# Kernel tuning notes

Hardware: AMD Instinct MI355X
Metric: run time of the kernel (lower is better)

## Reference

```python
import jax, jax.numpy as jnp
import numpy as np

HEADS = 16
DIM_HEAD = 64
LN_EPS = 1e-5
COS_EPS = 1e-8


def setup_inputs() -> dict:
    key = jax.random.key(0)
    ks = jax.random.split(key, 5)
    dim = 1024
    inner = HEADS * DIM_HEAD
    q = jax.random.normal(ks[0], (4, 1024, dim), dtype=jnp.float32)
    k = jax.random.normal(ks[1], (4, 2048, dim), dtype=jnp.float32)
    v = jax.random.normal(ks[2], (4, 2048, dim), dtype=jnp.float32)
    W_in = jax.random.normal(ks[3], (dim, inner), dtype=jnp.float32) * (1.0 / np.sqrt(dim))
    W_out = jax.random.normal(ks[4], (inner, dim), dtype=jnp.float32) * (1.0 / np.sqrt(inner))
    ln_gamma = jnp.ones((dim,), dtype=jnp.float32)
    ln_beta = jnp.zeros((dim,), dtype=jnp.float32)
    b_out = jnp.zeros((dim,), dtype=jnp.float32)
    return {"q": q, "k": k, "v": v, "ln_gamma": ln_gamma, "ln_beta": ln_beta,
            "W_in": W_in, "W_out": W_out, "b_out": b_out}


def _layernorm(x, gamma, beta):
    mu = jnp.mean(x, axis=-1, keepdims=True)
    var = jnp.mean(jnp.square(x - mu), axis=-1, keepdims=True)  # biased, as torch
    return (x - mu) * jax.lax.rsqrt(var + LN_EPS) * gamma + beta


def _project(t, gamma, beta, W_in):
    # LayerNorm -> Linear(no bias) -> split heads: b n (h d) -> b h n d
    x = _layernorm(t, gamma, beta) @ W_in
    b, n, _ = x.shape
    return x.reshape(b, n, HEADS, DIM_HEAD).transpose(0, 2, 1, 3)


def reference(q, k, v, ln_gamma, ln_beta, W_in, W_out, b_out):
    f_q = _project(q, ln_gamma, ln_beta, W_in)  # [b,h,n,d]
    f_k = _project(k, ln_gamma, ln_beta, W_in)  # [b,h,m,d]
    f_v = _project(v, ln_gamma, ln_beta, W_in)  # [b,h,m,d]
    dots = jnp.einsum('bhnd,bhmd->bhnm', f_q, f_k)
    qn = jnp.linalg.norm(f_q, axis=-1, keepdims=True)          # [b,h,n,1]
    kn = jnp.linalg.norm(f_k, axis=-1, keepdims=True)          # [b,h,m,1]
    attn = dots / (qn * kn.transpose(0, 1, 3, 2) + COS_EPS)    # [b,h,n,m]
    out = jnp.einsum('bhnm,bhmd->bhnd', attn, f_v)             # [b,h,n,d]
    b, h, n, d = out.shape
    out = out.transpose(0, 2, 1, 3).reshape(b, n, h * d)       # b n (h d)
    return out @ W_out + b_out
```

## Files before the change

### kernel.cpp

```cpp
#include <hip/hip_runtime.h>

constexpr int BATCH = 4;
constexpr int SEQQ  = 1024;
constexpr int SEQK  = 2048;
constexpr int DIM   = 1024;
constexpr int NH    = 16;
constexpr int DH    = 64;
constexpr int RQ    = BATCH * SEQQ;
constexpr int RK    = BATCH * SEQK;
constexpr int RTOT  = RQ + 2 * RK;
constexpr int BH    = BATCH * NH;
constexpr int NSLC  = 8;
constexpr float LN_EPS = 1e-5f;

typedef _Float16 f16;
typedef __attribute__((ext_vector_type(8))) _Float16 f16x8;
typedef __attribute__((ext_vector_type(4))) float f32x4;

__device__ __forceinline__ void async16(const void* g, void* l) {
  __builtin_amdgcn_global_load_lds(
      (const __attribute__((address_space(1))) void*)g,
      (__attribute__((address_space(3))) void*)l, 16, 0, 0);
}

__global__ void __launch_bounds__(256) ln_to_f16(
    const float* __restrict__ q, const float* __restrict__ k,
    const float* __restrict__ v, const float* __restrict__ gamma,
    const float* __restrict__ beta, f16* __restrict__ a_h) {
  const int row = blockIdx.x * 4 + (threadIdx.x >> 6);
  const int lane = threadIdx.x & 63;
  const float* src;
  if (row < RQ)            src = q + (size_t)row * DIM;
  else if (row < RQ + RK)  src = k + (size_t)(row - RQ) * DIM;
  else                     src = v + (size_t)(row - RQ - RK) * DIM;
  float4 x[4];
  float s = 0.f, s2 = 0.f;
#pragma unroll
  for (int c = 0; c < 4; c++) {
    x[c] = ((const float4*)src)[c * 64 + lane];
    s  += x[c].x + x[c].y + x[c].z + x[c].w;
    s2 += x[c].x * x[c].x + x[c].y * x[c].y + x[c].z * x[c].z + x[c].w * x[c].w;
  }
#pragma unroll
  for (int off = 1; off < 64; off <<= 1) {
    s  += __shfl_xor(s, off);
    s2 += __shfl_xor(s2, off);
  }
  const float mu = s / DIM;
  const float rs = rsqrtf(s2 / DIM - mu * mu + LN_EPS);
#pragma unroll
  for (int c = 0; c < 4; c++) {
    float4 g = ((const float4*)gamma)[c * 64 + lane];
    float4 b = ((const float4*)beta)[c * 64 + lane];
    union { f16 h[4]; uint2 u; } o;
    o.h[0] = (f16)((x[c].x - mu) * rs * g.x + b.x);
    o.h[1] = (f16)((x[c].y - mu) * rs * g.y + b.y);
    o.h[2] = (f16)((x[c].z - mu) * rs * g.z + b.z);
    o.h[3] = (f16)((x[c].w - mu) * rs * g.w + b.w);
    ((uint2*)(a_h + (size_t)row * DIM))[c * 64 + lane] = o.u;
  }
}

__global__ void __launch_bounds__(256) transpose_f16(
    const float* __restrict__ W0, const float* __restrict__ W1,
    f16* __restrict__ T0, f16* __restrict__ T1) {
  const float* W = blockIdx.z ? W1 : W0;
  f16* T = blockIdx.z ? T1 : T0;
  __shared__ float tile[32][33];
  int tx = threadIdx.x & 31, ty = threadIdx.x >> 5;
  int k0 = blockIdx.x * 32, n0 = blockIdx.y * 32;
#pragma unroll
  for (int i = 0; i < 4; i++)
    tile[ty + 8 * i][tx] = W[(size_t)(k0 + ty + 8 * i) * DIM + n0 + tx];
  __syncthreads();
#pragma unroll
  for (int i = 0; i < 4; i++)
    T[(size_t)(n0 + ty + 8 * i) * DIM + k0 + tx] = (f16)tile[tx][ty + 8 * i];
}

constexpr int PT_A = 320 * 64;
constexpr int PT_B = 256 * 64;

#define STAGE_A(buf, kt) do {                                        \
    const f16* s_ = gA + (size_t)(kt) * 64;                          \
    f16* d_ = AsW + (buf) * PT_A;                                    \
    async16(s_,          d_);                                        \
    async16(s_ +  65536, d_ + 4096);                                 \
    async16(s_ + 131072, d_ + 8192);                                 \
    async16(s_ + 196608, d_ + 12288);                                \
    async16(s_ + 262144, d_ + 16384);                                \
  } while (0)

#define STAGE_B(buf, kt) do {                                        \
    const f16* s_ = gB + (size_t)(kt) * 64;                          \
    f16* d_ = BsW + (buf) * PT_B;                                    \
    async16(s_,          d_);                                        \
    async16(s_ +  65536, d_ + 4096);                                 \
    async16(s_ + 131072, d_ + 8192);                                 \
    async16(s_ + 196608, d_ + 12288);                                \
  } while (0)

#define STAGE_AB(buf, kt) do { STAGE_A(buf, kt); STAGE_B(buf, kt); } while (0)

#define WT9 asm volatile("s_waitcnt vmcnt(9)" ::: "memory")
#define WT0 asm volatile("s_waitcnt vmcnt(0)" ::: "memory")
#define STN ((void)0)

#define HALF(BUF, H)                                                 \
    _Pragma("unroll") for (int j_ = 0; j_ < 4; ++j_)                 \
      bf[j_] = *(const f16x8*)(bB##H + (BUF) * PT_B + j_ * 1024);    \
    _Pragma("unroll") for (int f_ = 0; f_ < 5; ++f_)                 \
      af0[f_] = *(const f16x8*)(aB##H + (BUF) * PT_A + f_ * 1024);   \
    _Pragma("unroll") for (int f_ = 0; f_ < 5; ++f_)                 \
      af1[f_] = *(const f16x8*)(aB##H + (BUF) * PT_A + 5120 +        \
                                f_ * 1024);                          \
    __builtin_amdgcn_s_setprio(1);                                   \
    _Pragma("unroll") for (int f_ = 0; f_ < 5; ++f_)                 \
      _Pragma("unroll") for (int j_ = 0; j_ < 4; ++j_)               \
        acc[f_][j_] = __builtin_amdgcn_mfma_f32_16x16x32_f16(        \
            af0[f_], bf[j_], acc[f_][j_], 0, 0, 0);                  \
    _Pragma("unroll") for (int f_ = 0; f_ < 5; ++f_)                 \
      _Pragma("unroll") for (int j_ = 0; j_ < 4; ++j_)               \
        acc[5 + f_][j_] = __builtin_amdgcn_mfma_f32_16x16x32_f16(    \
            af1[f_], bf[j_], acc[5 + f_][j_], 0, 0, 0);              \
    __builtin_amdgcn_s_setprio(0);

#define PHT(BUF, STG, WT) {                                          \
    STG;                                                             \
    __builtin_amdgcn_sched_barrier(0);                               \
    WT;                                                              \
    __builtin_amdgcn_s_barrier();                                    \
    __builtin_amdgcn_sched_barrier(0);                               \
    HALF(BUF, 0)                                                     \
    HALF(BUF, 1)                                                     \
    __builtin_amdgcn_sched_barrier(0);                               \
    __builtin_amdgcn_s_barrier();                                    \
  }

__global__ void __launch_bounds__(512, 2) proj_gemm(
    const f16* __restrict__ A, const f16* __restrict__ Bt,
    f16* __restrict__ C) {
  __shared__ __align__(16) f16 As[2 * PT_A];
  __shared__ __align__(16) f16 Bs[2 * PT_B];

  const int tid = threadIdx.x;
  const int wid = tid >> 6;
  const int lane = tid & 63;
  const int la15 = lane & 15;

  const int bid = blockIdx.x;
  const int swz = (bid & 7) * 32 + (bid >> 3);
  const int row0 = (swz >> 2) * 320;
  const int col0 = (swz & 3) * 256;

  const int wm = (wid >> 2) * 160;
  const int wn = (wid & 3) * 64;

  const int hs = (tid & 7) ^ ((tid >> 3) & 7);
  const f16* gA = A + (size_t)(row0 + (tid >> 3)) * DIM + (hs >> 2) * 32 +
                  (hs & 3) * 8;
  const f16* gB = Bt + (size_t)(col0 + (tid >> 3)) * DIM + (hs >> 2) * 32 +
                  (hs & 3) * 8;
  f16* AsW = As + wid * 512;
  f16* BsW = Bs + wid * 512;

  const int g = lane >> 4;
  const int r7 = la15 & 7;
  const int cs0 = (g ^ r7) * 8;
  const int cs1 = ((4 + g) ^ r7) * 8;
  const f16* aB0 = As + (wm + la15) * 64 + cs0;
  const f16* aB1 = As + (wm + la15) * 64 + cs1;
  const f16* bB0 = Bs + (wn + la15) * 64 + cs0;
  const f16* bB1 = Bs + (wn + la15) * 64 + cs1;

  f32x4 acc[10][4];
#pragma unroll
  for (int i = 0; i < 10; i++)
#pragma unroll
    for (int j = 0; j < 4; j++) acc[i][j] = (f32x4){0.f, 0.f, 0.f, 0.f};
  f16x8 af0[5], af1[5], bf[4];

  STAGE_AB(0, 0);
  __builtin_amdgcn_sched_barrier(0);
  WT0;
  __builtin_amdgcn_s_barrier();
  __builtin_amdgcn_sched_barrier(0);

#pragma unroll 1
  for (int it = 0; it < 7; ++it) {
    const int t1 = 2 * it + 1, t2 = 2 * it + 2;
    PHT(0, STAGE_AB(1, t1), WT9)
    PHT(1, STAGE_AB(0, t2), WT9)
  }
  PHT(0, STAGE_AB(1, 15), WT9)
  PHT(1, STN,             WT0)

  const int crow = (lane >> 4) * 4;
#pragma unroll
  for (int mh = 0; mh < 2; ++mh)
#pragma unroll
    for (int f = 0; f < 5; ++f) {
      const int m = mh * 5 + f;
      const int rbase = row0 + wm + mh * 80 + f * 16 + crow;
#pragma unroll
      for (int r = 0; r < 4; ++r) {
        float s = acc[m][0][r] * acc[m][0][r] + acc[m][1][r] * acc[m][1][r]
                + acc[m][2][r] * acc[m][2][r] + acc[m][3][r] * acc[m][3][r];
        s += __shfl_xor(s, 1);
        s += __shfl_xor(s, 2);
        s += __shfl_xor(s, 4);
        s += __shfl_xor(s, 8);
        if (rbase + r < RQ + RK) {
          const float inv = rsqrtf(s);
#pragma unroll
          for (int j = 0; j < 4; ++j) acc[m][j][r] *= inv;
        }
      }
    }

  f16* sc = As;
  const int wmi = wid >> 2;
  const int ehalf = tid >> 8;
  const int err = (tid >> 4) & 15;
  const int ecc = tid & 15;
  const f16* rb_l = sc + ehalf * (16 * 264) + err * 264 + ecc * 16;
#pragma unroll
  for (int mh = 0; mh < 2; ++mh)
#pragma unroll
    for (int f = 0; f < 5; ++f) {
      const int m = mh * 5 + f;
#pragma unroll
      for (int j = 0; j < 4; ++j)
#pragma unroll
        for (int r = 0; r < 4; ++r)
          sc[wmi * (16 * 264) + (crow + r) * 264 + wn + j * 16 + la15] =
              (f16)acc[m][j][r];
      __syncthreads();
      f16x8 v0 = *(const f16x8*)(rb_l);
      f16x8 v1 = *(const f16x8*)(rb_l + 8);
      const int grow = row0 + ehalf * 160 + mh * 80 + f * 16 + err;
      f16* Cp = C + (size_t)grow * DIM + col0 + ecc * 16;
      *(f16x8*)(Cp) = v0;
      *(f16x8*)(Cp + 8) = v1;
      if (!(mh == 1 && f == 4)) __syncthreads();
    }
}

template <int MT, bool OUT_F16, bool NORMS, bool BIAS, bool PERB>
__global__ void __launch_bounds__(256) mfma_gemm(
    const f16* __restrict__ A, const f16* __restrict__ Bt,
    void* __restrict__ Cout, const float* __restrict__ bias) {
  constexpr int JT = (MT == 128) ? 4 : 2;
  __shared__ f16 Asl[2][MT * 32];
  __shared__ f16 Bsl[2][128 * 32];
  const int t = threadIdx.x;
  const int wid = t >> 6;
  const int lane = t & 63;
  const int row0 = blockIdx.x * MT;
  const int col0 = blockIdx.y * 128;
  const int wm = (MT == 128) ? (wid >> 1) * 64 : 0;
  const int wn = (MT == 128) ? (wid & 1) * 64 : wid * 32;

  const f16* BtB = PERB ? Bt + (size_t)(row0 >> 10) * DIM * DIM : Bt;

  const int rB = 32 * wid + (lane >> 2);
  const int qB = ((lane & 3) - ((rB >> 1) & 3)) & 3;
  const f16* gB = BtB + (size_t)(col0 + rB) * DIM + qB * 8;
  f16* lB0 = Bsl[0] + 32 * wid * 32;
  f16* lB1 = Bsl[1] + 32 * wid * 32;
  const int rA = (MT == 128 ? 32 : 16) * wid + (lane >> 2);
  const int qA = ((lane & 3) - ((rA >> 1) & 3)) & 3;
  const f16* gA = A + (size_t)(row0 + rA) * DIM + qA * 8;
  f16* lA0 = Asl[0] + (MT == 128 ? 32 : 16) * wid * 32;
  f16* lA1 = Asl[1] + (MT == 128 ? 32 : 16) * wid * 32;

  f32x4 acc[4][JT];
#pragma unroll
  for (int i = 0; i < 4; i++)
#pragma unroll
    for (int j = 0; j < JT; j++) acc[i][j] = (f32x4){0.f, 0.f, 0.f, 0.f};

  const int mrow = lane & 15;
  const int kq_p = (((lane >> 4) + ((lane >> 1) & 3)) & 3) * 8;

  for (int kt = 0; kt < DIM / 64; ++kt) {
    if (kt) __syncthreads();
    const int ko = kt * 64;
    async16(gA + ko,      lA0);
    if (MT == 128) async16(gA + ko + 16 * DIM, lA0 + 512);
    async16(gB + ko,      lB0);
    async16(gB + ko + 16 * DIM, lB0 + 512);
    async16(gA + ko + 32, lA1);
    if (MT == 128) async16(gA + ko + 32 + 16 * DIM, lA1 + 512);
    async16(gB + ko + 32, lB1);
    async16(gB + ko + 32 + 16 * DIM, lB1 + 512);
    __syncthreads();

#pragma unroll
    for (int h = 0; h < 2; ++h) {
      f16x8 af[4], bf[JT];
#pragma unroll
      for (int i = 0; i < 4; i++)
        af[i] = *(const f16x8*)(Asl[h] + (wm + i * 16 + mrow) * 32 + kq_p);
#pragma unroll
      for (int j = 0; j < JT; j++)
        bf[j] = *(const f16x8*)(Bsl[h] + (wn + j * 16 + mrow) * 32 + kq_p);
#pragma unroll
      for (int i = 0; i < 4; i++)
#pragma unroll
        for (int j = 0; j < JT; j++)
          acc[i][j] = __builtin_amdgcn_mfma_f32_16x16x32_f16(af[i], bf[j], acc[i][j], 0, 0, 0);
    }
  }

  if (NORMS && MT == 128) {
    if (row0 < RQ + RK) {
      float sums[4][4];
#pragma unroll
      for (int i = 0; i < 4; i++)
#pragma unroll
        for (int r = 0; r < 4; r++) {
          float s = 0.f;
#pragma unroll
          for (int j = 0; j < JT; j++) s += acc[i][j][r] * acc[i][j][r];
          sums[i][r] = s;
        }
#pragma unroll
      for (int off = 1; off < 16; off <<= 1)
#pragma unroll
        for (int i = 0; i < 4; i++)
#pragma unroll
          for (int r = 0; r < 4; r++)
            sums[i][r] += __shfl_xor(sums[i][r], off);
#pragma unroll
      for (int i = 0; i < 4; i++)
#pragma unroll
        for (int r = 0; r < 4; r++) {
          const float inv = rsqrtf(sums[i][r]);
#pragma unroll
          for (int j = 0; j < JT; j++) acc[i][j][r] *= inv;
        }
    }
  }

  const int ccol = lane & 15;
  const int crow = (lane >> 4) * 4;
  if (OUT_F16) {
    f16* C = (f16*)Cout;
#pragma unroll
    for (int j = 0; j < JT; j++) {
      const int col = col0 + wn + j * 16 + ccol;
#pragma unroll
      for (int i = 0; i < 4; i++) {
        f16* Cp = C + (size_t)(row0 + wm + i * 16 + crow) * DIM + col;
#pragma unroll
        for (int r = 0; r < 4; r++) Cp[(size_t)r * DIM] = (f16)acc[i][j][r];
      }
    }
  } else {
    float* C = (float*)Cout;
#pragma unroll
    for (int j = 0; j < JT; j++) {
      const int col = col0 + wn + j * 16 + ccol;
      float bv = BIAS ? bias[col] : 0.f;
#pragma unroll
      for (int i = 0; i < 4; i++) {
        float* Cp = C + (size_t)(row0 + wm + i * 16 + crow) * DIM + col;
#pragma unroll
        for (int r = 0; r < 4; r++) Cp[(size_t)r * DIM] = acc[i][j][r] + bv;
      }
    }
  }
}

__global__ void __launch_bounds__(256) s_kernel(
    const f16* __restrict__ f, float* __restrict__ S4) {
  const int bh = blockIdx.x;
  const int b = bh >> 4, h = bh & 15;
  const int mbase = blockIdx.y * (SEQK / NSLC);
  const int t = threadIdx.x;
  __shared__ float ks[32][68];
  __shared__ float vs[32][68];
  const int lm   = t >> 3;
  const int lseg = (t & 7) * 8;
  const int d1 = (t & 15) * 4;
  const int d2 = (t >> 4) * 4;
  float acc[4][4] = {{0.f}};
  const f16* fk_base = f + ((size_t)RQ + (size_t)b * SEQK) * DIM + h * DH;
  const f16* fv_base = f + ((size_t)RQ + RK + (size_t)b * SEQK) * DIM + h * DH;

  int m = mbase + lm;
  f16x8 kv = *(const f16x8*)(fk_base + (size_t)m * DIM + lseg);
  f16x8 vv = *(const f16x8*)(fv_base + (size_t)m * DIM + lseg);

  constexpr int SUBS = SEQK / NSLC / 32;
  for (int sub = 0; sub < SUBS; ++sub) {
    __syncthreads();
#pragma unroll
    for (int e = 0; e < 8; e++) {
      ks[lm][lseg + e] = (float)kv[e];
      vs[lm][lseg + e] = (float)vv[e];
    }
    __syncthreads();
    if (sub + 1 < SUBS) {
      m = mbase + (sub + 1) * 32 + lm;
      kv = *(const f16x8*)(fk_base + (size_t)m * DIM + lseg);
      vv = *(const f16x8*)(fv_base + (size_t)m * DIM + lseg);
    }
#pragma unroll
    for (int mm = 0; mm < 32; ++mm) {
      float4 kk = *(const float4*)&ks[mm][d1];
      float4 vv2 = *(const float4*)&vs[mm][d2];
      acc[0][0] = fmaf(kk.x, vv2.x, acc[0][0]);
      acc[0][1] = fmaf(kk.x, vv2.y, acc[0][1]);
      acc[0][2] = fmaf(kk.x, vv2.z, acc[0][2]);
      acc[0][3] = fmaf(kk.x, vv2.w, acc[0][3]);
      acc[1][0] = fmaf(kk.y, vv2.x, acc[1][0]);
      acc[1][1] = fmaf(kk.y, vv2.y, acc[1][1]);
      acc[1][2] = fmaf(kk.y, vv2.z, acc[1][2]);
      acc[1][3] = fmaf(kk.y, vv2.w, acc[1][3]);
      acc[2][0] = fmaf(kk.z, vv2.x, acc[2][0]);
      acc[2][1] = fmaf(kk.z, vv2.y, acc[2][1]);
      acc[2][2] = fmaf(kk.z, vv2.z, acc[2][2]);
      acc[2][3] = fmaf(kk.z, vv2.w, acc[2][3]);
      acc[3][0] = fmaf(kk.w, vv2.x, acc[3][0]);
      acc[3][1] = fmaf(kk.w, vv2.y, acc[3][1]);
      acc[3][2] = fmaf(kk.w, vv2.z, acc[3][2]);
      acc[3][3] = fmaf(kk.w, vv2.w, acc[3][3]);
    }
  }
  float* Sp = S4 + ((size_t)blockIdx.y * BH + bh) * DH * DH;
#pragma unroll
  for (int i = 0; i < 4; i++)
#pragma unroll
    for (int j = 0; j < 4; j++)
      Sp[(d1 + i) * DH + (d2 + j)] = acc[i][j];
}

__global__ void __launch_bounds__(256) s_reduce(
    const float* __restrict__ S4, f16* __restrict__ Sh) {
  const int bh = blockIdx.x;
  const int t = threadIdx.x;
  const size_t base = (size_t)bh * DH * DH + t * 16;
  constexpr size_t STR = (size_t)BH * DH * DH;
#pragma unroll
  for (int c = 0; c < 4; c++) {
    float4 s = {0.f, 0.f, 0.f, 0.f};
#pragma unroll
    for (int p = 0; p < NSLC; p++) {
      float4 sp = *(const float4*)(S4 + base + p * STR + 4 * c);
      s.x += sp.x; s.y += sp.y; s.z += sp.z; s.w += sp.w;
    }
    union { f16 h[4]; uint2 u; } o;
    o.h[0] = (f16)s.x; o.h[1] = (f16)s.y; o.h[2] = (f16)s.z; o.h[3] = (f16)s.w;
    *(uint2*)(Sh + base + 4 * c) = o.u;
  }
}

__global__ void __launch_bounds__(256) m_build(
    const f16* __restrict__ wt_out, const f16* __restrict__ Sh,
    f16* __restrict__ Mt) {
  const int n0 = blockIdx.x * 128;
  const int bh = blockIdx.y;
  const int b = bh >> 4, h = bh & 15;
  __shared__ f16 Asl[128 * 64];
  __shared__ f16 Bsl[64 * 64];
  const int t = threadIdx.x;
  const int wid = t >> 6, lane = t & 63;

  const f16* gA = wt_out + (size_t)(n0 + 32 * wid + (lane >> 3)) * DIM
                  + 64 * h + (lane & 7) * 8;
  f16* lA = Asl + 32 * wid * 64;
  const f16* gB = Sh + (size_t)bh * DH * DH + (16 * wid + (lane >> 3)) * 64
                  + (lane & 7) * 8;
  f16* lB = Bsl + 16 * wid * 64;
#pragma unroll
  for (int o = 0; o < 4; o++) async16(gA + (size_t)(8 * o) * DIM, lA + 8 * o * 64);
  async16(gB, lB);
  async16(gB + 8 * 64, lB + 8 * 64);
  __syncthreads();

  const int wm = (wid >> 1) * 64;
  const int wn = (wid & 1) * 32;
  const int mrow = lane & 15;
  f32x4 acc[4][2];
#pragma unroll
  for (int i = 0; i < 4; i++)
#pragma unroll
    for (int j = 0; j < 2; j++) acc[i][j] = (f32x4){0.f, 0.f, 0.f, 0.f};

#pragma unroll
  for (int kh = 0; kh < 2; kh++) {
    const int kq = kh * 32 + (lane >> 4) * 8;
    f16x8 af[4], bf[2];
#pragma unroll
    for (int i = 0; i < 4; i++)
      af[i] = *(const f16x8*)(Asl + (wm + i * 16 + mrow) * 64 + kq);
#pragma unroll
    for (int j = 0; j < 2; j++)
      bf[j] = *(const f16x8*)(Bsl + (wn + j * 16 + mrow) * 64 + kq);
#pragma unroll
    for (int i = 0; i < 4; i++)
#pragma unroll
      for (int j = 0; j < 2; j++)
        acc[i][j] = __builtin_amdgcn_mfma_f32_16x16x32_f16(af[i], bf[j], acc[i][j], 0, 0, 0);
  }

  const int ccol = lane & 15;
  const int crow = (lane >> 4) * 4;
  f16* Mb = Mt + (size_t)b * DIM * DIM;
#pragma unroll
  for (int j = 0; j < 2; j++) {
    const int col = 64 * h + wn + j * 16 + ccol;
#pragma unroll
    for (int i = 0; i < 4; i++) {
      f16* Mp = Mb + (size_t)(n0 + wm + i * 16 + crow) * DIM + col;
#pragma unroll
      for (int r = 0; r < 4; r++) Mp[(size_t)r * DIM] = (f16)acc[i][j][r];
    }
  }
}

extern "C" void kernel_launch(void* const* d_in, const int* in_sizes, int n_in,
                              void* d_out, int out_size, void* d_ws, size_t ws_size,
                              hipStream_t stream) {
  const float* q     = (const float*)d_in[0];
  const float* k     = (const float*)d_in[1];
  const float* v     = (const float*)d_in[2];
  const float* gamma = (const float*)d_in[3];
  const float* beta  = (const float*)d_in[4];
  const float* W_in  = (const float*)d_in[5];
  const float* W_out = (const float*)d_in[6];
  const float* b_out = (const float*)d_in[7];
  float* out = (float*)d_out;

  char* w = (char*)d_ws;
  f16*   f      = (f16*)w;
  f16*   a_h    = f + (size_t)RTOT * DIM;
  f16*   wt_in  = a_h + (size_t)RTOT * DIM;
  f16*   wt_out = wt_in + (size_t)DIM * DIM;
  f16*   Mt     = wt_out + (size_t)DIM * DIM;
  f16*   Sh     = Mt + (size_t)BATCH * DIM * DIM;
  float* S4     = (float*)(Sh + (size_t)BH * DH * DH);

  ln_to_f16<<<RTOT / 4, 256, 0, stream>>>(q, k, v, gamma, beta, a_h);
  transpose_f16<<<dim3(DIM / 32, DIM / 32, 2), 256, 0, stream>>>(
      W_in, W_out, wt_in, wt_out);

  proj_gemm<<<dim3(256), 512, 0, stream>>>(a_h, wt_in, f);

  s_kernel<<<dim3(BH, NSLC), 256, 0, stream>>>(f, S4);

  s_reduce<<<BH, 256, 0, stream>>>(S4, Sh);

  m_build<<<dim3(DIM / 128, BH), 256, 0, stream>>>(wt_out, Sh, Mt);

  mfma_gemm<64, false, false, true, true>
      <<<dim3(RQ / 64, DIM / 128), 256, 0, stream>>>(f, Mt, out, b_out);
}
```

Measured before the change: 231.7 us.

## Merge LN and transpose kernels, restructure GEMM pipeline, add dedicated final GEMM

Fuses the LayerNorm-to-f16 kernel and the weight transpose into one launch, which removes a kernel launch and lets both run concurrently. Reorders the barrier and wait structure in the projection GEMM so the next tile's async load is issued after the barrier and fully drained after compute, dropping the partial vmcnt(9) wait. Replaces the generic templated final GEMM with a specialized 512-thread, 128x128-tile kernel that uses double-buffered async LDS staging and a swizzled block order. The full vmcnt(0) wait after each tile could expose load latency that the earlier partial wait had hidden.

```diff
diff --git a/kernel.cpp b/kernel.cpp
--- a/kernel.cpp
+++ b/kernel.cpp
@@ -23,59 +23,61 @@
       (__attribute__((address_space(3))) void*)l, 16, 0, 0);
 }
 
-__global__ void __launch_bounds__(256) ln_to_f16(
+__global__ void __launch_bounds__(256) pre_kernel(
     const float* __restrict__ q, const float* __restrict__ k,
     const float* __restrict__ v, const float* __restrict__ gamma,
-    const float* __restrict__ beta, f16* __restrict__ a_h) {
-  const int row = blockIdx.x * 4 + (threadIdx.x >> 6);
-  const int lane = threadIdx.x & 63;
-  const float* src;
-  if (row < RQ)            src = q + (size_t)row * DIM;
-  else if (row < RQ + RK)  src = k + (size_t)(row - RQ) * DIM;
-  else                     src = v + (size_t)(row - RQ - RK) * DIM;
-  float4 x[4];
-  float s = 0.f, s2 = 0.f;
-#pragma unroll
-  for (int c = 0; c < 4; c++) {
-    x[c] = ((const float4*)src)[c * 64 + lane];
-    s  += x[c].x + x[c].y + x[c].z + x[c].w;
-    s2 += x[c].x * x[c].x + x[c].y * x[c].y + x[c].z * x[c].z + x[c].w * x[c].w;
-  }
-#pragma unroll
-  for (int off = 1; off < 64; off <<= 1) {
-    s  += __shfl_xor(s, off);
-    s2 += __shfl_xor(s2, off);
-  }
-  const float mu = s / DIM;
-  const float rs = rsqrtf(s2 / DIM - mu * mu + LN_EPS);
-#pragma unroll
-  for (int c = 0; c < 4; c++) {
-    float4 g = ((const float4*)gamma)[c * 64 + lane];
-    float4 b = ((const float4*)beta)[c * 64 + lane];
-    union { f16 h[4]; uint2 u; } o;
-    o.h[0] = (f16)((x[c].x - mu) * rs * g.x + b.x);
-    o.h[1] = (f16)((x[c].y - mu) * rs * g.y + b.y);
-    o.h[2] = (f16)((x[c].z - mu) * rs * g.z + b.z);
-    o.h[3] = (f16)((x[c].w - mu) * rs * g.w + b.w);
-    ((uint2*)(a_h + (size_t)row * DIM))[c * 64 + lane] = o.u;
-  }
-}
-
-__global__ void __launch_bounds__(256) transpose_f16(
+    const float* __restrict__ beta, f16* __restrict__ a_h,
     const float* __restrict__ W0, const float* __restrict__ W1,
     f16* __restrict__ T0, f16* __restrict__ T1) {
-  const float* W = blockIdx.z ? W1 : W0;
-  f16* T = blockIdx.z ? T1 : T0;
   __shared__ float tile[32][33];
-  int tx = threadIdx.x & 31, ty = threadIdx.x >> 5;
-  int k0 = blockIdx.x * 32, n0 = blockIdx.y * 32;
-#pragma unroll
-  for (int i = 0; i < 4; i++)
-    tile[ty + 8 * i][tx] = W[(size_t)(k0 + ty + 8 * i) * DIM + n0 + tx];
-  __syncthreads();
-#pragma unroll
-  for (int i = 0; i < 4; i++)
-    T[(size_t)(n0 + ty + 8 * i) * DIM + k0 + tx] = (f16)tile[tx][ty + 8 * i];
+  if (blockIdx.x < RTOT / 4) {
+    const int row = blockIdx.x * 4 + (threadIdx.x >> 6);
+    const int lane = threadIdx.x & 63;
+    const float* src;
+    if (row < RQ)            src = q + (size_t)row * DIM;
+    else if (row < RQ + RK)  src = k + (size_t)(row - RQ) * DIM;
+    else                     src = v + (size_t)(row - RQ - RK) * DIM;
+    float4 x[4];
+    float s = 0.f, s2 = 0.f;
+#pragma unroll
+    for (int c = 0; c < 4; c++) {
+      x[c] = ((const float4*)src)[c * 64 + lane];
+      s  += x[c].x + x[c].y + x[c].z + x[c].w;
+      s2 += x[c].x * x[c].x + x[c].y * x[c].y + x[c].z * x[c].z + x[c].w * x[c].w;
+    }
+#pragma unroll
+    for (int off = 1; off < 64; off <<= 1) {
+      s  += __shfl_xor(s, off);
+      s2 += __shfl_xor(s2, off);
+    }
+    const float mu = s / DIM;
+    const float rs = rsqrtf(s2 / DIM - mu * mu + LN_EPS);
+#pragma unroll
+    for (int c = 0; c < 4; c++) {
+      float4 g = ((const float4*)gamma)[c * 64 + lane];
+      float4 b = ((const float4*)beta)[c * 64 + lane];
+      union { f16 h[4]; uint2 u; } o;
+      o.h[0] = (f16)((x[c].x - mu) * rs * g.x + b.x);
+      o.h[1] = (f16)((x[c].y - mu) * rs * g.y + b.y);
+      o.h[2] = (f16)((x[c].z - mu) * rs * g.z + b.z);
+      o.h[3] = (f16)((x[c].w - mu) * rs * g.w + b.w);
+      ((uint2*)(a_h + (size_t)row * DIM))[c * 64 + lane] = o.u;
+    }
+  } else {
+    const int tz = blockIdx.x - RTOT / 4;
+    const float* W = (tz >= 1024) ? W1 : W0;
+    f16* T = (tz >= 1024) ? T1 : T0;
+    const int rem = tz & 1023;
+    const int k0 = (rem & 31) * 32, n0 = (rem >> 5) * 32;
+    int tx = threadIdx.x & 31, ty = threadIdx.x >> 5;
+#pragma unroll
+    for (int i = 0; i < 4; i++)
+      tile[ty + 8 * i][tx] = W[(size_t)(k0 + ty + 8 * i) * DIM + n0 + tx];
+    __syncthreads();
+#pragma unroll
+    for (int i = 0; i < 4; i++)
+      T[(size_t)(n0 + ty + 8 * i) * DIM + k0 + tx] = (f16)tile[tx][ty + 8 * i];
+  }
 }
 
 constexpr int PT_A = 320 * 64;
@@ -102,8 +104,8 @@
 
 #define STAGE_AB(buf, kt) do { STAGE_A(buf, kt); STAGE_B(buf, kt); } while (0)
 
-#define WT9 asm volatile("s_waitcnt vmcnt(9)" ::: "memory")
 #define WT0 asm volatile("s_waitcnt vmcnt(0)" ::: "memory")
+#define WTN ((void)0)
 #define STN ((void)0)
 
 #define HALF(BUF, H)                                                 \
@@ -125,16 +127,14 @@
             af1[f_], bf[j_], acc[5 + f_][j_], 0, 0, 0);              \
     __builtin_amdgcn_s_setprio(0);
 
-#define PHT(BUF, STG, WT) {                                          \
-    STG;                                                             \
-    __builtin_amdgcn_sched_barrier(0);                               \
-    WT;                                                              \
+#define PTILE(BUF, STG, TVW) {                                       \
     __builtin_amdgcn_s_barrier();                                    \
     __builtin_amdgcn_sched_barrier(0);                               \
+    STG;                                                             \
     HALF(BUF, 0)                                                     \
     HALF(BUF, 1)                                                     \
     __builtin_amdgcn_sched_barrier(0);                               \
-    __builtin_amdgcn_s_barrier();                                    \
+    TVW;                                                             \
   }
 
 __global__ void __launch_bounds__(512, 2) proj_gemm(
@@ -183,17 +183,15 @@
   STAGE_AB(0, 0);
   __builtin_amdgcn_sched_barrier(0);
   WT0;
-  __builtin_amdgcn_s_barrier();
-  __builtin_amdgcn_sched_barrier(0);
 
 #pragma unroll 1
   for (int it = 0; it < 7; ++it) {
     const int t1 = 2 * it + 1, t2 = 2 * it + 2;
-    PHT(0, STAGE_AB(1, t1), WT9)
-    PHT(1, STAGE_AB(0, t2), WT9)
-  }
-  PHT(0, STAGE_AB(1, 15), WT9)
-  PHT(1, STN,             WT0)
+    PTILE(0, STAGE_AB(1, t1), WT0)
+    PTILE(1, STAGE_AB(0, t2), WT0)
+  }
+  PTILE(0, STAGE_AB(1, 15), WT0)
+  PTILE(1, STN, WTN)
 
   const int crow = (lane >> 4) * 4;
 #pragma unroll
@@ -244,133 +242,6 @@
       *(f16x8*)(Cp + 8) = v1;
       if (!(mh == 1 && f == 4)) __syncthreads();
     }
-}
-
-template <int MT, bool OUT_F16, bool NORMS, bool BIAS, bool PERB>
-__global__ void __launch_bounds__(256) mfma_gemm(
-    const f16* __restrict__ A, const f16* __restrict__ Bt,
-    void* __restrict__ Cout, const float* __restrict__ bias) {
-  constexpr int JT = (MT == 128) ? 4 : 2;
-  __shared__ f16 Asl[2][MT * 32];
-  __shared__ f16 Bsl[2][128 * 32];
-  const int t = threadIdx.x;
-  const int wid = t >> 6;
-  const int lane = t & 63;
-  const int row0 = blockIdx.x * MT;
-  const int col0 = blockIdx.y * 128;
-  const int wm = (MT == 128) ? (wid >> 1) * 64 : 0;
-  const int wn = (MT == 128) ? (wid & 1) * 64 : wid * 32;
-
-  const f16* BtB = PERB ? Bt + (size_t)(row0 >> 10) * DIM * DIM : Bt;
-
-  const int rB = 32 * wid + (lane >> 2);
-  const int qB = ((lane & 3) - ((rB >> 1) & 3)) & 3;
-  const f16* gB = BtB + (size_t)(col0 + rB) * DIM + qB * 8;
-  f16* lB0 = Bsl[0] + 32 * wid * 32;
-  f16* lB1 = Bsl[1] + 32 * wid * 32;
-  const int rA = (MT == 128 ? 32 : 16) * wid + (lane >> 2);
-  const int qA = ((lane & 3) - ((rA >> 1) & 3)) & 3;
-  const f16* gA = A + (size_t)(row0 + rA) * DIM + qA * 8;
-  f16* lA0 = Asl[0] + (MT == 128 ? 32 : 16) * wid * 32;
-  f16* lA1 = Asl[1] + (MT == 128 ? 32 : 16) * wid * 32;
-
-  f32x4 acc[4][JT];
-#pragma unroll
-  for (int i = 0; i < 4; i++)
-#pragma unroll
-    for (int j = 0; j < JT; j++) acc[i][j] = (f32x4){0.f, 0.f, 0.f, 0.f};
-
-  const int mrow = lane & 15;
-  const int kq_p = (((lane >> 4) + ((lane >> 1) & 3)) & 3) * 8;
-
-  for (int kt = 0; kt < DIM / 64; ++kt) {
-    if (kt) __syncthreads();
-    const int ko = kt * 64;
-    async16(gA + ko,      lA0);
-    if (MT == 128) async16(gA + ko + 16 * DIM, lA0 + 512);
-    async16(gB + ko,      lB0);
-    async16(gB + ko + 16 * DIM, lB0 + 512);
-    async16(gA + ko + 32, lA1);
-    if (MT == 128) async16(gA + ko + 32 + 16 * DIM, lA1 + 512);
-    async16(gB + ko + 32, lB1);
-    async16(gB + ko + 32 + 16 * DIM, lB1 + 512);
-    __syncthreads();
-
-#pragma unroll
-    for (int h = 0; h < 2; ++h) {
-      f16x8 af[4], bf[JT];
-#pragma unroll
-      for (int i = 0; i < 4; i++)
-        af[i] = *(const f16x8*)(Asl[h] + (wm + i * 16 + mrow) * 32 + kq_p);
-#pragma unroll
-      for (int j = 0; j < JT; j++)
-        bf[j] = *(const f16x8*)(Bsl[h] + (wn + j * 16 + mrow) * 32 + kq_p);
-#pragma unroll
-      for (int i = 0; i < 4; i++)
-#pragma unroll
-        for (int j = 0; j < JT; j++)
-          acc[i][j] = __builtin_amdgcn_mfma_f32_16x16x32_f16(af[i], bf[j], acc[i][j], 0, 0, 0);
-    }
-  }
-
-  if (NORMS && MT == 128) {
-    if (row0 < RQ + RK) {
-      float sums[4][4];
-#pragma unroll
-      for (int i = 0; i < 4; i++)
-#pragma unroll
-        for (int r = 0; r < 4; r++) {
-          float s = 0.f;
-#pragma unroll
-          for (int j = 0; j < JT; j++) s += acc[i][j][r] * acc[i][j][r];
-          sums[i][r] = s;
-        }
-#pragma unroll
-      for (int off = 1; off < 16; off <<= 1)
-#pragma unroll
-        for (int i = 0; i < 4; i++)
-#pragma unroll
-          for (int r = 0; r < 4; r++)
-            sums[i][r] += __shfl_xor(sums[i][r], off);
-#pragma unroll
-      for (int i = 0; i < 4; i++)
-#pragma unroll
-        for (int r = 0; r < 4; r++) {
-          const float inv = rsqrtf(sums[i][r]);
-#pragma unroll
-          for (int j = 0; j < JT; j++) acc[i][j][r] *= inv;
-        }
-    }
-  }
-
-  const int ccol = lane & 15;
-  const int crow = (lane >> 4) * 4;
-  if (OUT_F16) {
-    f16* C = (f16*)Cout;
-#pragma unroll
-    for (int j = 0; j < JT; j++) {
-      const int col = col0 + wn + j * 16 + ccol;
-#pragma unroll
-      for (int i = 0; i < 4; i++) {
-        f16* Cp = C + (size_t)(row0 + wm + i * 16 + crow) * DIM + col;
-#pragma unroll
-        for (int r = 0; r < 4; r++) Cp[(size_t)r * DIM] = (f16)acc[i][j][r];
-      }
-    }
-  } else {
-    float* C = (float*)Cout;
-#pragma unroll
-    for (int j = 0; j < JT; j++) {
-      const int col = col0 + wn + j * 16 + ccol;
-      float bv = BIAS ? bias[col] : 0.f;
-#pragma unroll
-      for (int i = 0; i < 4; i++) {
-        float* Cp = C + (size_t)(row0 + wm + i * 16 + crow) * DIM + col;
-#pragma unroll
-        for (int r = 0; r < 4; r++) Cp[(size_t)r * DIM] = acc[i][j][r] + bv;
-      }
-    }
-  }
 }
 
 __global__ void __launch_bounds__(256) s_kernel(
@@ -521,6 +392,111 @@
   }
 }
 
+constexpr int FT_SZ = 128 * 64;
+
+#define FSTG(P, gp, kt, buf) do {                                    \
+    const f16* s_ = (gp) + (size_t)(kt) * 64;                        \
+    f16* d_ = (P) + (buf) * FT_SZ;                                   \
+    async16(s_,         d_);                                         \
+    async16(s_ + 65536, d_ + 4096);                                  \
+  } while (0)
+
+#define FHALF(BUF, H)                                                \
+    _Pragma("unroll") for (int j_ = 0; j_ < 2; ++j_)                 \
+      gbf[j_] = *(const f16x8*)(bB##H + (BUF) * FT_SZ + j_ * 1024);  \
+    _Pragma("unroll") for (int i_ = 0; i_ < 4; ++i_)                 \
+      gaf[i_] = *(const f16x8*)(aB##H + (BUF) * FT_SZ + i_ * 1024);  \
+    __builtin_amdgcn_s_setprio(1);                                   \
+    _Pragma("unroll") for (int i_ = 0; i_ < 4; ++i_)                 \
+      _Pragma("unroll") for (int j_ = 0; j_ < 2; ++j_)               \
+        facc[i_][j_] = __builtin_amdgcn_mfma_f32_16x16x32_f16(       \
+            gaf[i_], gbf[j_], facc[i_][j_], 0, 0, 0);                \
+    __builtin_amdgcn_s_setprio(0);
+
+#define FTILE(BUF, STG, TVW) {                                       \
+    __builtin_amdgcn_s_barrier();                                    \
+    __builtin_amdgcn_sched_barrier(0);                               \
+    STG;                                                             \
+    FHALF(BUF, 0)                                                    \
+    FHALF(BUF, 1)                                                    \
+    __builtin_amdgcn_sched_barrier(0);                               \
+    TVW;                                                             \
+  }
+
+__global__ void __launch_bounds__(512, 2) fin_gemm(
+    const f16* __restrict__ f, const f16* __restrict__ Mt,
+    const float* __restrict__ bias, float* __restrict__ out) {
+  __shared__ __align__(16) f16 As[2 * FT_SZ];
+  __shared__ __align__(16) f16 Bs[2 * FT_SZ];
+  const int tid = threadIdx.x;
+  const int wid = tid >> 6;
+  const int lane = tid & 63;
+  const int la15 = lane & 15;
+
+  const int bid = blockIdx.x;
+  const int swz = (bid & 7) * 32 + (bid >> 3);
+  const int b  = swz >> 6;
+  const int rt = (swz >> 3) & 7;
+  const int ct = swz & 7;
+  const int grow0 = b * SEQQ + rt * 128;
+  const int col0 = ct * 128;
+
+  const int wm = (wid >> 2) * 64;
+  const int wn = (wid & 3) * 32;
+
+  const int hs = (tid & 7) ^ ((tid >> 3) & 7);
+  const f16* gA = f + (size_t)(grow0 + (tid >> 3)) * DIM + (hs >> 2) * 32 +
+                  (hs & 3) * 8;
+  const f16* gB = Mt + (size_t)b * DIM * DIM +
+                  (size_t)(col0 + (tid >> 3)) * DIM + (hs >> 2) * 32 +
+                  (hs & 3) * 8;
+  f16* AsW = As + wid * 512;
+  f16* BsW = Bs + wid * 512;
+
+  const int g = lane >> 4;
+  const int r7 = la15 & 7;
+  const int cs0 = (g ^ r7) * 8;
+  const int cs1 = ((4 + g) ^ r7) * 8;
+  const f16* aB0 = As + (wm + la15) * 64 + cs0;
+  const f16* aB1 = As + (wm + la15) * 64 + cs1;
+  const f16* bB0 = Bs + (wn + la15) * 64 + cs0;
+  const f16* bB1 = Bs + (wn + la15) * 64 + cs1;
+
+  f32x4 facc[4][2];
+#pragma unroll
+  for (int i = 0; i < 4; i++)
+#pragma unroll
+    for (int j = 0; j < 2; j++) facc[i][j] = (f32x4){0.f, 0.f, 0.f, 0.f};
+  f16x8 gaf[4], gbf[2];
+
+  FSTG(AsW, gA, 0, 0);
+  FSTG(BsW, gB, 0, 0);
+  __builtin_amdgcn_sched_barrier(0);
+  WT0;
+
+#pragma unroll 1
+  for (int it = 0; it < 7; ++it) {
+    const int t1 = 2 * it + 1, t2 = 2 * it + 2;
+    FTILE(0, { FSTG(AsW, gA, t1, 1); FSTG(BsW, gB, t1, 1); }, WT0)
+    FTILE(1, { FSTG(AsW, gA, t2, 0); FSTG(BsW, gB, t2, 0); }, WT0)
+  }
+  FTILE(0, { FSTG(AsW, gA, 15, 1); FSTG(BsW, gB, 15, 1); }, WT0)
+  FTILE(1, STN, WTN)
+
+  const int crow = (lane >> 4) * 4;
+#pragma unroll
+  for (int j = 0; j < 2; ++j) {
+    const int col = col0 + wn + j * 16 + la15;
+    const float bv = bias[col];
+#pragma unroll
+    for (int i = 0; i < 4; ++i) {
+      float* Op = out + (size_t)(grow0 + wm + i * 16 + crow) * DIM + col;
+#pragma unroll
+      for (int r = 0; r < 4; ++r) Op[(size_t)r * DIM] = facc[i][j][r] + bv;
+    }
+  }
+}
+
 extern "C" void kernel_launch(void* const* d_in, const int* in_sizes, int n_in,
                               void* d_out, int out_size, void* d_ws, size_t ws_size,
                               hipStream_t stream) {
@@ -543,9 +519,8 @@
   f16*   Sh     = Mt + (size_t)BATCH * DIM * DIM;
   float* S4     = (float*)(Sh + (size_t)BH * DH * DH);
 
-  ln_to_f16<<<RTOT / 4, 256, 0, stream>>>(q, k, v, gamma, beta, a_h);
-  transpose_f16<<<dim3(DIM / 32, DIM / 32, 2), 256, 0, stream>>>(
-      W_in, W_out, wt_in, wt_out);
+  pre_kernel<<<RTOT / 4 + 2048, 256, 0, stream>>>(
+      q, k, v, gamma, beta, a_h, W_in, W_out, wt_in, wt_out);
 
   proj_gemm<<<dim3(256), 512, 0, stream>>>(a_h, wt_in, f);
 
@@ -555,6 +530,5 @@
 
   m_build<<<dim3(DIM / 128, BH), 256, 0, stream>>>(wt_out, Sh, Mt);
 
-  mfma_gemm<64, false, false, true, true>
-      <<<dim3(RQ / 64, DIM / 128), 256, 0, stream>>>(f, Mt, out, b_out);
-}
+  fin_gemm<<<dim3(256), 512, 0, stream>>>(f, Mt, b_out, out);
+}
```

Result: no change. 229.0 us (-1.1%).
